# Kernel tuning notes

Measured on AMD Instinct MI355X. Metric: run time of the kernel, lower is better.

The kernel has to match this reference:

```python
import jax, jax.numpy as jnp
import numpy as np

L = 7
LVL = 3
B = 8
R = 16
N = 4 ** L  # 16384
P = N // 4  # number of local blocks
T = 4 * R   # ConvLocal output features


def build_permutation_indices(L, l):
    delta = 4 ** (L - l - 1)
    tmp = np.tile(np.arange(4) * delta, delta)
    tmp += np.repeat(np.arange(delta), 4)
    tmp = np.tile(tmp, 4 ** l)
    tmp += np.repeat(np.arange(4 ** l) * 4 ** (L - l), 4 ** (L - l))
    return jnp.asarray(tmp, dtype=jnp.int32)


def setup_inputs() -> dict:
    key = jax.random.key(0)
    kx, k1, k2, k3, k4 = jax.random.split(key, 5)
    scale = 1.0 / np.sqrt(T)
    x = jax.random.normal(kx, (B, 2, N, R), dtype=jnp.float32)
    # flax ConvLocal kernels: (out_spatial, kernel_size*in_features, features)
    W_rr = jax.random.normal(k1, (P, 4 * R, T), dtype=jnp.float32) * scale
    W_ri = jax.random.normal(k2, (P, 4 * R, T), dtype=jnp.float32) * scale
    W_ir = jax.random.normal(k3, (P, 4 * R, T), dtype=jnp.float32) * scale
    W_ii = jax.random.normal(k4, (P, 4 * R, T), dtype=jnp.float32) * scale
    perm_idx = build_permutation_indices(L, LVL)
    return {"x": x, "W_rr": W_rr, "W_ri": W_ri, "W_ir": W_ir,
            "W_ii": W_ii, "perm_idx": perm_idx}


def reference(x, W_rr, W_ri, W_ir, W_ii, perm_idx):
    b, _, n, r = x.shape
    p = n // 4
    # butterfly permutation gather along the spatial axis
    xp = jnp.take(x, perm_idx, axis=2)            # [B, 2, n, r]
    # group into length-4 windows; flax ConvLocal flattens (kernel, in_feat)
    xr = xp[:, 0].reshape(b, p, 4 * r)            # [B, p, 4r]
    xi = xp[:, 1].reshape(b, p, 4 * r)
    # block-diagonal (locally connected) matmuls, complex-style combine
    y_re = jnp.einsum('bpi,pio->bpo', xr, W_rr) + jnp.einsum('bpi,pio->bpo', xi, W_ri)
    y_im = jnp.einsum('bpi,pio->bpo', xr, W_ir) + jnp.einsum('bpi,pio->bpo', xi, W_ii)
    y = jnp.stack([y_re, y_im], axis=1)           # [B, 2, p, 4r]
    return y.reshape(b, 2, n, r)
```

## Files before the change

### kernel.cpp

```cpp
#include <hip/hip_runtime.h>

#define C_N 16384
#define C_R 16
#define C_P 4096
#define C_B 8

__global__ __launch_bounds__(64, 4)
void butterfly_local_conv(const float* __restrict__ x,
                          const float* __restrict__ Wrr,
                          const float* __restrict__ Wri,
                          const float* __restrict__ Wir,
                          const float* __restrict__ Wii,
                          const int*   __restrict__ perm,
                          float* __restrict__ out)
{
    __shared__ float xs[2][C_B][64];

    const int lane = threadIdx.x;
    const int p    = blockIdx.x;

    const int sc = lane >> 5;
    const int sb = (lane >> 2) & 7;
    const int ss = lane & 3;
    const int n  = perm[4 * p + ss];
    const float4* xsrc = (const float4*)(x + (((size_t)(sb * 2 + sc)) * C_N + n) * C_R);
    const float4 v0 = xsrc[0], v1 = xsrc[1], v2 = xsrc[2], v3 = xsrc[3];

    const size_t wbase = (size_t)p * 64 * 64 + lane;
    const float* __restrict__ prr = Wrr + wbase;
    const float* __restrict__ pri = Wri + wbase;
    const float* __restrict__ pir = Wir + wbase;
    const float* __restrict__ pii = Wii + wbase;

    float buf0[32], buf1[32];
    #pragma unroll
    for (int k = 0; k < 8; ++k) {
        buf0[k]      = prr[k * 64];
        buf0[8 + k]  = pri[k * 64];
        buf0[16 + k] = pir[k * 64];
        buf0[24 + k] = pii[k * 64];
    }

    {
        float4* dst = (float4*)(&xs[sc][sb][ss * 16]);
        dst[0] = v0; dst[1] = v1; dst[2] = v2; dst[3] = v3;
    }

    float acc_re[C_B], acc_im[C_B];
    #pragma unroll
    for (int b = 0; b < C_B; ++b) { acc_re[b] = 0.0f; acc_im[b] = 0.0f; }

    #pragma unroll
    for (int ch = 0; ch < 8; ++ch) {
        float* cur = (ch & 1) ? buf1 : buf0;
        float* nxt = (ch & 1) ? buf0 : buf1;
        if (ch < 7) {
            const int ib = (ch + 1) * 8;
            #pragma unroll
            for (int k = 0; k < 8; ++k) {
                nxt[k]      = prr[(ib + k) * 64];
                nxt[8 + k]  = pri[(ib + k) * 64];
                nxt[16 + k] = pir[(ib + k) * 64];
                nxt[24 + k] = pii[(ib + k) * 64];
            }
        }
        const int i0 = ch * 8;
        #pragma unroll
        for (int b = 0; b < C_B; ++b) {
            float xr[8], xi[8];
            *(float4*)&xr[0] = *(const float4*)(&xs[0][b][i0]);
            *(float4*)&xr[4] = *(const float4*)(&xs[0][b][i0 + 4]);
            *(float4*)&xi[0] = *(const float4*)(&xs[1][b][i0]);
            *(float4*)&xi[4] = *(const float4*)(&xs[1][b][i0 + 4]);
            #pragma unroll
            for (int k = 0; k < 8; ++k) {
                acc_re[b] = fmaf(xr[k], cur[k],      acc_re[b]);
                acc_re[b] = fmaf(xi[k], cur[8 + k],  acc_re[b]);
                acc_im[b] = fmaf(xr[k], cur[16 + k], acc_im[b]);
                acc_im[b] = fmaf(xi[k], cur[24 + k], acc_im[b]);
            }
        }
    }

    const size_t obase = (size_t)p * 64 + lane;
    #pragma unroll
    for (int b = 0; b < C_B; ++b) {
        out[((size_t)(b * 2 + 0)) * (C_N * C_R) + obase] = acc_re[b];
        out[((size_t)(b * 2 + 1)) * (C_N * C_R) + obase] = acc_im[b];
    }
}

extern "C" void kernel_launch(void* const* d_in, const int* in_sizes, int n_in,
                              void* d_out, int out_size, void* d_ws, size_t ws_size,
                              hipStream_t stream) {
    const float* x    = (const float*)d_in[0];
    const float* Wrr  = (const float*)d_in[1];
    const float* Wri  = (const float*)d_in[2];
    const float* Wir  = (const float*)d_in[3];
    const float* Wii  = (const float*)d_in[4];
    const int*   perm = (const int*)d_in[5];
    float* out = (float*)d_out;

    butterfly_local_conv<<<dim3(C_P), dim3(64), 0, stream>>>(
        x, Wrr, Wri, Wir, Wii, perm, out);
}
```

Before: 273.2 us.

## Stage weights into LDS via direct global-to-LDS loads and split work across waves

Each block now handles one output half (re or im) for one local block, with 256 threads split across four waves that each compute two batch rows. Weights are copied straight into shared memory with global_load_lds 16-byte transfers instead of strided per-lane register loads, and x is fetched one float4 per thread. The aim is more memory-level parallelism and more waves in flight on this bandwidth-bound kernel. In exchange, x is loaded twice (once per half), a block barrier is added, and 32 KB of LDS per block may limit occupancy.

```diff
diff --git a/kernel.cpp b/kernel.cpp
--- a/kernel.cpp
+++ b/kernel.cpp
@@ -1,11 +1,12 @@
 #include <hip/hip_runtime.h>
+#include <stdint.h>
 
 #define C_N 16384
 #define C_R 16
 #define C_P 4096
 #define C_B 8
 
-__global__ __launch_bounds__(64, 4)
+__global__ __launch_bounds__(256)
 void butterfly_local_conv(const float* __restrict__ x,
                           const float* __restrict__ Wrr,
                           const float* __restrict__ Wri,
@@ -14,80 +15,80 @@
                           const int*   __restrict__ perm,
                           float* __restrict__ out)
 {
+    __shared__ float lw[2][64][64];
     __shared__ float xs[2][C_B][64];
 
-    const int lane = threadIdx.x;
-    const int p    = blockIdx.x;
+    const int t    = threadIdx.x;
+    const int lane = t & 63;
+    const int w    = t >> 6;
+    const int p    = blockIdx.x >> 1;
+    const int half = blockIdx.x & 1;
 
-    const int sc = lane >> 5;
-    const int sb = (lane >> 2) & 7;
-    const int ss = lane & 3;
+    const float* __restrict__ WA = half ? Wir : Wrr;
+    const float* __restrict__ WB = half ? Wii : Wri;
+
+    const int sc = t >> 7;
+    const int sb = (t >> 4) & 7;
+    const int ss = (t >> 2) & 3;
+    const int sq = t & 3;
     const int n  = perm[4 * p + ss];
-    const float4* xsrc = (const float4*)(x + (((size_t)(sb * 2 + sc)) * C_N + n) * C_R);
-    const float4 v0 = xsrc[0], v1 = xsrc[1], v2 = xsrc[2], v3 = xsrc[3];
+    const float4 xv =
+        ((const float4*)(x + (((size_t)(sb * 2 + sc)) * C_N + n) * C_R))[sq];
 
-    const size_t wbase = (size_t)p * 64 * 64 + lane;
-    const float* __restrict__ prr = Wrr + wbase;
-    const float* __restrict__ pri = Wri + wbase;
-    const float* __restrict__ pir = Wir + wbase;
-    const float* __restrict__ pii = Wii + wbase;
-
-    float buf0[32], buf1[32];
-    #pragma unroll
-    for (int k = 0; k < 8; ++k) {
-        buf0[k]      = prr[k * 64];
-        buf0[8 + k]  = pri[k * 64];
-        buf0[16 + k] = pir[k * 64];
-        buf0[24 + k] = pii[k * 64];
+    {
+        const float* Wsrc = (w < 2) ? WA : WB;
+        const int    mat  = (w < 2) ? 0 : 1;
+        const int    row0 = (w & 1) * 32;
+        const float* gbase = Wsrc + (size_t)p * 4096 + (size_t)row0 * 64 + lane * 4;
+        const float* lbase = &lw[mat][row0][0];
+        #pragma unroll
+        for (int j = 0; j < 8; ++j) {
+            __builtin_amdgcn_global_load_lds(
+                (const __attribute__((address_space(1))) uint32_t*)(gbase + j * 256),
+                (__attribute__((address_space(3))) uint32_t*)((char*)lbase + j * 1024),
+                16, 0, 0);
+        }
     }
 
-    {
-        float4* dst = (float4*)(&xs[sc][sb][ss * 16]);
-        dst[0] = v0; dst[1] = v1; dst[2] = v2; dst[3] = v3;
-    }
+    *(float4*)(&xs[sc][sb][ss * 16 + sq * 4]) = xv;
 
-    float acc_re[C_B], acc_im[C_B];
-    #pragma unroll
-    for (int b = 0; b < C_B; ++b) { acc_re[b] = 0.0f; acc_im[b] = 0.0f; }
+    __syncthreads();
+
+    const int b0 = w * 2;
+    float acc0 = 0.0f, acc1 = 0.0f;
 
     #pragma unroll
-    for (int ch = 0; ch < 8; ++ch) {
-        float* cur = (ch & 1) ? buf1 : buf0;
-        float* nxt = (ch & 1) ? buf0 : buf1;
-        if (ch < 7) {
-            const int ib = (ch + 1) * 8;
-            #pragma unroll
-            for (int k = 0; k < 8; ++k) {
-                nxt[k]      = prr[(ib + k) * 64];
-                nxt[8 + k]  = pri[(ib + k) * 64];
-                nxt[16 + k] = pir[(ib + k) * 64];
-                nxt[24 + k] = pii[(ib + k) * 64];
-            }
+    for (int i0 = 0; i0 < 64; i0 += 8) {
+        float wa[8], wb[8];
+        #pragma unroll
+        for (int k = 0; k < 8; ++k) {
+            wa[k] = lw[0][i0 + k][lane];
+            wb[k] = lw[1][i0 + k][lane];
         }
-        const int i0 = ch * 8;
+        float xr[8], xi[8];
+        *(float4*)&xr[0] = *(const float4*)(&xs[0][b0][i0]);
+        *(float4*)&xr[4] = *(const float4*)(&xs[0][b0][i0 + 4]);
+        *(float4*)&xi[0] = *(const float4*)(&xs[1][b0][i0]);
+        *(float4*)&xi[4] = *(const float4*)(&xs[1][b0][i0 + 4]);
         #pragma unroll
-        for (int b = 0; b < C_B; ++b) {
-            float xr[8], xi[8];
-            *(float4*)&xr[0] = *(const float4*)(&xs[0][b][i0]);
-            *(float4*)&xr[4] = *(const float4*)(&xs[0][b][i0 + 4]);
-            *(float4*)&xi[0] = *(const float4*)(&xs[1][b][i0]);
-            *(float4*)&xi[4] = *(const float4*)(&xs[1][b][i0 + 4]);
-            #pragma unroll
-            for (int k = 0; k < 8; ++k) {
-                acc_re[b] = fmaf(xr[k], cur[k],      acc_re[b]);
-                acc_re[b] = fmaf(xi[k], cur[8 + k],  acc_re[b]);
-                acc_im[b] = fmaf(xr[k], cur[16 + k], acc_im[b]);
-                acc_im[b] = fmaf(xi[k], cur[24 + k], acc_im[b]);
-            }
+        for (int k = 0; k < 8; ++k) {
+            acc0 = fmaf(xr[k], wa[k], acc0);
+            acc0 = fmaf(xi[k], wb[k], acc0);
+        }
+        *(float4*)&xr[0] = *(const float4*)(&xs[0][b0 + 1][i0]);
+        *(float4*)&xr[4] = *(const float4*)(&xs[0][b0 + 1][i0 + 4]);
+        *(float4*)&xi[0] = *(const float4*)(&xs[1][b0 + 1][i0]);
+        *(float4*)&xi[4] = *(const float4*)(&xs[1][b0 + 1][i0 + 4]);
+        #pragma unroll
+        for (int k = 0; k < 8; ++k) {
+            acc1 = fmaf(xr[k], wa[k], acc1);
+            acc1 = fmaf(xi[k], wb[k], acc1);
         }
     }
 
     const size_t obase = (size_t)p * 64 + lane;
-    #pragma unroll
-    for (int b = 0; b < C_B; ++b) {
-        out[((size_t)(b * 2 + 0)) * (C_N * C_R) + obase] = acc_re[b];
-        out[((size_t)(b * 2 + 1)) * (C_N * C_R) + obase] = acc_im[b];
-    }
+    out[((size_t)(b0 * 2 + half)) * (C_N * C_R) + obase] = acc0;
+    out[((size_t)((b0 + 1) * 2 + half)) * (C_N * C_R) + obase] = acc1;
 }
 
 extern "C" void kernel_launch(void* const* d_in, const int* in_sizes, int n_in,
@@ -101,6 +102,6 @@
     const int*   perm = (const int*)d_in[5];
     float* out = (float*)d_out;
 
-    butterfly_local_conv<<<dim3(C_P), dim3(64), 0, stream>>>(
+    butterfly_local_conv<<<dim3(C_P * 2), dim3(256), 0, stream>>>(
         x, Wrr, Wri, Wir, Wii, perm, out);
 }
```

Result: faster. 261.6 us (-4.3%).
